# Kernel optimization log

Measured on AMD Instinct MI355X. Metric: run time of the kernel, lower is better.

The kernel has to match this reference:

```python
import jax, jax.numpy as jnp
import numpy as np

B, S, L, D, M = 32, 256, 64, 100, 20  # batch, n_sentences, max_sentence_len, embed_dim, n_memories


def setup_inputs() -> dict:
    key = jax.random.key(0)
    ks = jax.random.split(key, 6)
    batch = jax.random.normal(ks[0], (B, S, L, D), dtype=jnp.float32)
    enc_mult = jnp.ones((L, D), dtype=jnp.float32)  # input_encoder_multiplier (init to ones)
    keys = 0.1 * jax.random.normal(ks[1], (M, D), dtype=jnp.float32)
    U = 0.1 * jax.random.normal(ks[2], (D, D), dtype=jnp.float32)  # nn.Linear weight [out,in]
    V = 0.1 * jax.random.normal(ks[3], (D, D), dtype=jnp.float32)
    W = 0.1 * jax.random.normal(ks[4], (D, D), dtype=jnp.float32)
    prelu_a = jnp.ones((), dtype=jnp.float32)  # PReLU(init=1), single shared parameter
    return {"batch": batch, "enc_mult": enc_mult, "keys": keys, "U": U, "V": V, "W": W, "prelu_a": prelu_a}


def reference(batch, enc_mult, keys, U, V, W, prelu_a):
    # Encode: elementwise multiply by learned positional multiplier, sum over words -> [B, S, D]
    enc = (batch * enc_mult).sum(axis=2)

    def prelu(x):
        return jnp.where(x >= 0, x, prelu_a * x)

    # keys @ V.T is step-invariant
    keysV = jnp.einsum('md,ed->me', keys, V)  # [M, D]

    def step(mem, s):  # mem: [B, M, D], s: [B, D]
        memory_gate = jnp.einsum('bd,bmd->bm', s, mem)          # [B, M]
        key_gate = jnp.einsum('bd,md->bm', s, keys)              # [B, M]
        gate = jax.nn.sigmoid(memory_gate + key_gate)            # [B, M]
        cand = prelu(
            jnp.einsum('bmd,ed->bme', mem, U)                    # U(memories)
            + keysV[None, :, :]                                  # V(keys)
            + jnp.einsum('bd,ed->be', s, W)[:, None, :]          # W(sentence), broadcast over M
        )
        mem = mem + cand * gate[:, :, None]
        mem = mem / jnp.linalg.norm(mem, axis=2, keepdims=True)  # L2 normalize each memory slot
        return mem, None

    mem0 = jnp.broadcast_to(keys[None, :, :], (B, M, D))  # memories init = keys repeated per batch
    mem_final, _ = jax.lax.scan(step, mem0, jnp.swapaxes(enc, 0, 1))  # scan over sentences
    return mem_final
```

## Files before the change

### kernel.cpp

```cpp
#include <hip/hip_runtime.h>


typedef float v2f __attribute__((ext_vector_type(2)));

__global__ __launch_bounds__(320) void encode_k(
    const float* __restrict__ batch,
    const float* __restrict__ encm,
    float* __restrict__ enc)
{
    __shared__ float prod[6400];
    __shared__ float part[200];
    const int t = threadIdx.x;
    const int row = blockIdx.x;
    const float4* rb = (const float4*)batch + (size_t)row * 1600;
    const float4* e4 = (const float4*)encm;
    float4* p4 = (float4*)prod;
    #pragma unroll
    for (int i = 0; i < 5; ++i) {
        const int idx = i * 320 + t;
        float4 x = rb[idx];
        float4 mu = e4[idx];
        float4 p;
        p.x = x.x * mu.x; p.y = x.y * mu.y; p.z = x.z * mu.z; p.w = x.w * mu.w;
        p4[idx] = p;
    }
    __syncthreads();
    if (t < 200) {
        const int c = (t < 100) ? t : (t - 100);
        const int l0 = (t < 100) ? 0 : 32;
        float s0 = 0.f, s1 = 0.f;
        #pragma unroll
        for (int l = 0; l < 32; l += 2) {
            s0 += prod[(l0 + l) * 100 + c];
            s1 += prod[(l0 + l + 1) * 100 + c];
        }
        part[t] = s0 + s1;
    }
    __syncthreads();
    if (t < 100) enc[(size_t)row * 100 + t] = part[t] + part[100 + t];
}

__global__ void prep_k(const float* __restrict__ W,
                       const float* __restrict__ keys,
                       float* __restrict__ T)
{
    const int d = blockIdx.x;
    const int e = threadIdx.x;
    float v = 0.f;
    if (e < 100) v = W[e * 100 + d];
    else if (e < 120) v = keys[(e - 100) * 100 + d];
    T[d * 128 + e] = v;
}

__global__ __launch_bounds__(128) void project_k(
    const float* __restrict__ enc,
    const float* __restrict__ T,
    float* __restrict__ sWp,
    float* __restrict__ kg)
{
    __shared__ float encS[400];
    const int t = threadIdx.x;
    const int row0 = blockIdx.x * 4;
    if (t < 100) ((float4*)encS)[t] = ((const float4*)(enc + (size_t)row0 * 100))[t];
    __syncthreads();
    float a0 = 0.f, a1 = 0.f, a2 = 0.f, a3 = 0.f;
    #pragma unroll 4
    for (int d = 0; d < 100; ++d) {
        const float w = T[d * 128 + t];
        a0 += w * encS[d];
        a1 += w * encS[100 + d];
        a2 += w * encS[200 + d];
        a3 += w * encS[300 + d];
    }
    if (t < 100) {
        sWp[(size_t)row0 * 100 + t]       = a0;
        sWp[(size_t)(row0 + 1) * 100 + t] = a1;
        sWp[(size_t)(row0 + 2) * 100 + t] = a2;
        sWp[(size_t)(row0 + 3) * 100 + t] = a3;
    } else if (t < 120) {
        const int m = t - 100;
        kg[(size_t)row0 * 20 + m]       = a0;
        kg[(size_t)(row0 + 1) * 20 + m] = a1;
        kg[(size_t)(row0 + 2) * 20 + m] = a2;
        kg[(size_t)(row0 + 3) * 20 + m] = a3;
    }
}

template <int CTRL>
__device__ __forceinline__ float dpp_add_f(float x) {
    int s = __builtin_amdgcn_update_dpp(0, __float_as_int(x), CTRL, 0xF, 0xF, true);
    return x + __int_as_float(s);
}
__device__ __forceinline__ float lane63(float x) {
    return __int_as_float(__builtin_amdgcn_readlane(__float_as_int(x), 63));
}
#define DPP6(v) v = dpp_add_f<0x111>(v); v = dpp_add_f<0x112>(v); v = dpp_add_f<0x114>(v); \
                v = dpp_add_f<0x118>(v); v = dpp_add_f<0x142>(v); v = dpp_add_f<0x143>(v);

#define CAND_STORE(C0, C1) { cbuf[lane] = (C0); cbuf[64 + lane] = (C1); }

#define MATVEC_READ(RES)                                                \
    {                                                                   \
        v2f A0 = {0.f, 0.f}, A1 = {0.f, 0.f};                           \
        v2f A2 = {0.f, 0.f}, A3 = {0.f, 0.f};                           \
        _Pragma("unroll")                                               \
        for (int j = 0; j < 25; ++j) {                                  \
            float4 cc = cbuf4[j];                                       \
            v2f clo = {cc.x, cc.y};                                     \
            v2f chi = {cc.z, cc.w};                                     \
            A0 = __builtin_elementwise_fma(UE0[2 * j],     clo, A0);    \
            A1 = __builtin_elementwise_fma(UE0[2 * j + 1], chi, A1);    \
            A2 = __builtin_elementwise_fma(UE1[2 * j],     clo, A2);    \
            A3 = __builtin_elementwise_fma(UE1[2 * j + 1], chi, A3);    \
        }                                                               \
        v2f sA = A0 + A1, sB = A2 + A3;                                 \
        RES.x = sA.x + sA.y;                                            \
        RES.y = sB.x + sB.y;                                            \
    }

__global__ __attribute__((amdgpu_waves_per_eu(1, 1))) __launch_bounds__(64)
void entnet_scan(
    const float* __restrict__ enc,
    const float* __restrict__ sWp,
    const float* __restrict__ kg,
    const float* __restrict__ keys,
    const float* __restrict__ U,
    const float* __restrict__ V,
    const float* __restrict__ paPtr,
    float* __restrict__ out)
{
    __shared__ float4 cbuf4[32];
    float* cbuf = (float*)cbuf4;
    const int lane = threadIdx.x;
    const int xcd = blockIdx.x & 7;
    const int gg  = blockIdx.x >> 3;
    const int b = xcd * 4 + gg / 20;
    const int m = gg % 20;
    const bool hi = (lane < 36);
    const float h = hi ? 1.f : 0.f;
    const int e0 = lane;
    const int e1 = hi ? (64 + lane) : 99;
    const float pa = paPtr[0];

    v2f UE0[50], UE1[50];
    {
        const float4* u0 = (const float4*)(U + e0 * 100);
        const float4* u1 = (const float4*)(U + e1 * 100);
        #pragma unroll
        for (int k = 0; k < 25; ++k) {
            float4 a = u0[k], c = u1[k];
            UE0[2 * k]     = (v2f){a.x, a.y};
            UE0[2 * k + 1] = (v2f){a.z, a.w};
            UE1[2 * k]     = (v2f){c.x, c.y};
            UE1[2 * k + 1] = (v2f){c.z, c.w};
        }
    }

    float kv0 = 0.f, kv1 = 0.f;
    {
        const float4* km = (const float4*)(keys + m * 100);
        const float4* v0 = (const float4*)(V + e0 * 100);
        const float4* v1 = (const float4*)(V + e1 * 100);
        #pragma unroll
        for (int k = 0; k < 25; ++k) {
            float4 kk = km[k], a = v0[k], c = v1[k];
            kv0 += a.x * kk.x + a.y * kk.y + a.z * kk.z + a.w * kk.w;
            kv1 += c.x * kk.x + c.y * kk.y + c.z * kk.z + c.w * kk.w;
        }
    }
    const float k0 = keys[m * 100 + e0];
    const float k1 = h * keys[m * 100 + e1];
    float nm0 = k0, nm1 = k1;

    v2f P;
    CAND_STORE(k0, k1);
    MATVEC_READ(P);

    float nq = k0 * k0 + k1 * k1;
    DPP6(nq)
    float nsq = lane63(nq);
    float rn = 1.f;

    const float* encRow = enc + (size_t)b * 25600;
    const float* sWRow  = sWp + (size_t)b * 25600;
    const float* kgRow  = kg + (size_t)b * 5120 + m;

    float sw0 = sWRow[e0], sw1 = sWRow[e1];
    float g;
    {
        const float sv0 = encRow[e0], sv1 = encRow[e1];
        const float kg0 = kgRow[0];
        float q1 = sv0 * nm0 + sv1 * nm1;
        DPP6(q1)
        const float Q1 = lane63(q1);
        g = 1.f / (1.f + __expf(-(Q1 + kg0)));
    }

    for (int step = 0; step < 256; ++step) {
        const int nxt = (step < 255 ? step + 1 : 255);
        const float nsv0 = encRow[nxt * 100 + e0], nsv1 = encRow[nxt * 100 + e1];
        const float nsw0 = sWRow[nxt * 100 + e0], nsw1 = sWRow[nxt * 100 + e1];
        const float nkg  = kgRow[nxt * 20];

        const float x0 = rn * P.x + kv0 + sw0;
        const float x1 = rn * P.y + kv1 + sw1;
        float c0 = (x0 >= 0.f) ? x0 : pa * x0;
        float c1 = (x1 >= 0.f) ? x1 : pa * x1;
        c1 *= h;

        CAND_STORE(c0, c1);

        float q3 = nm0 * c0 + nm1 * c1;
        float p4 = c0 * c0 + c1 * c1;
        #define RND2(C) q3 = dpp_add_f<C>(q3); p4 = dpp_add_f<C>(p4);
        RND2(0x111) RND2(0x112) RND2(0x114) RND2(0x118) RND2(0x142) RND2(0x143)
        #undef RND2

        v2f Q;
        MATVEC_READ(Q);

        const float Q3 = lane63(q3);
        const float P4 = lane63(p4);
        const float n2 = nsq + 2.f * (g * rn) * Q3 + g * g * P4;
        const float rnn = rsqrtf(n2);
        nsq = 1.f;

        nm0 = rn * nm0 + g * c0;
        nm1 = rn * nm1 + g * c1;
        P.x = rn * P.x + g * Q.x;
        P.y = rn * P.y + g * Q.y;

        float q1 = nsv0 * nm0 + nsv1 * nm1;
        DPP6(q1)
        const float Q1 = lane63(q1);
        g = 1.f / (1.f + __expf(-(rnn * Q1 + nkg)));

        rn = rnn;
        sw0 = nsw0; sw1 = nsw1;
    }
    float* orow = out + (size_t)(b * 20 + m) * 100;
    orow[e0] = nm0 * rn;
    if (hi) orow[e1] = nm1 * rn;
}

extern "C" void kernel_launch(void* const* d_in, const int* in_sizes, int n_in,
                              void* d_out, int out_size, void* d_ws, size_t ws_size,
                              hipStream_t stream) {
    const float* batch = (const float*)d_in[0];
    const float* encm  = (const float*)d_in[1];
    const float* keys  = (const float*)d_in[2];
    const float* U     = (const float*)d_in[3];
    const float* V     = (const float*)d_in[4];
    const float* W     = (const float*)d_in[5];
    const float* pa    = (const float*)d_in[6];
    float* out = (float*)d_out;

    float* enc = (float*)d_ws;
    float* sWp = enc + 819200;
    float* kgb = sWp + 819200;
    float* T   = kgb + 163840;

    encode_k<<<8192, 320, 0, stream>>>(batch, encm, enc);
    prep_k<<<100, 128, 0, stream>>>(W, keys, T);
    project_k<<<2048, 128, 0, stream>>>(enc, T, sWp, kgb);
    entnet_scan<<<640, 64, 0, stream>>>(enc, sWp, kgb, keys, U, V, pa, out);
}
```

Before: 491.6 us.

## Process two memory slots per wave in scan kernel to halve block count

Each scan wave now carries two independent memory slots (m and m+10) instead of one. The U rows held in registers are reused for both matvecs, and the two independent dependency chains interleave, which hides the latency of DPP reductions and LDS accesses. The grid shrinks from 640 to 320 single-wave blocks. On 256 CUs that removes the partial second wave of blocks, but each wave does twice the work per step, so the serial chain length per wave goes up.

```diff
diff --git a/kernel.cpp b/kernel.cpp
--- a/kernel.cpp
+++ b/kernel.cpp
@@ -97,25 +97,29 @@
 #define DPP6(v) v = dpp_add_f<0x111>(v); v = dpp_add_f<0x112>(v); v = dpp_add_f<0x114>(v); \
                 v = dpp_add_f<0x118>(v); v = dpp_add_f<0x142>(v); v = dpp_add_f<0x143>(v);
 
-#define CAND_STORE(C0, C1) { cbuf[lane] = (C0); cbuf[64 + lane] = (C1); }
-
-#define MATVEC_READ(RES)                                                \
+#define MATVEC2(RA, RB)                                                 \
     {                                                                   \
-        v2f A0 = {0.f, 0.f}, A1 = {0.f, 0.f};                           \
-        v2f A2 = {0.f, 0.f}, A3 = {0.f, 0.f};                           \
+        v2f A0 = {0.f,0.f}, A1 = {0.f,0.f}, A2 = {0.f,0.f}, A3 = {0.f,0.f}; \
+        v2f B0 = {0.f,0.f}, B1 = {0.f,0.f}, B2 = {0.f,0.f}, B3 = {0.f,0.f}; \
         _Pragma("unroll")                                               \
         for (int j = 0; j < 25; ++j) {                                  \
-            float4 cc = cbuf4[j];                                       \
-            v2f clo = {cc.x, cc.y};                                     \
-            v2f chi = {cc.z, cc.w};                                     \
-            A0 = __builtin_elementwise_fma(UE0[2 * j],     clo, A0);    \
-            A1 = __builtin_elementwise_fma(UE0[2 * j + 1], chi, A1);    \
-            A2 = __builtin_elementwise_fma(UE1[2 * j],     clo, A2);    \
-            A3 = __builtin_elementwise_fma(UE1[2 * j + 1], chi, A3);    \
+            float4 ca = cbufA4[j];                                      \
+            float4 cb = cbufB4[j];                                      \
+            v2f calo = {ca.x, ca.y}, cahi = {ca.z, ca.w};               \
+            v2f cblo = {cb.x, cb.y}, cbhi = {cb.z, cb.w};               \
+            A0 = __builtin_elementwise_fma(UE0[2 * j],     calo, A0);   \
+            A1 = __builtin_elementwise_fma(UE0[2 * j + 1], cahi, A1);   \
+            A2 = __builtin_elementwise_fma(UE1[2 * j],     calo, A2);   \
+            A3 = __builtin_elementwise_fma(UE1[2 * j + 1], cahi, A3);   \
+            B0 = __builtin_elementwise_fma(UE0[2 * j],     cblo, B0);   \
+            B1 = __builtin_elementwise_fma(UE0[2 * j + 1], cbhi, B1);   \
+            B2 = __builtin_elementwise_fma(UE1[2 * j],     cblo, B2);   \
+            B3 = __builtin_elementwise_fma(UE1[2 * j + 1], cbhi, B3);   \
         }                                                               \
         v2f sA = A0 + A1, sB = A2 + A3;                                 \
-        RES.x = sA.x + sA.y;                                            \
-        RES.y = sB.x + sB.y;                                            \
+        RA.x = sA.x + sA.y;  RA.y = sB.x + sB.y;                        \
+        v2f tA = B0 + B1, tB = B2 + B3;                                 \
+        RB.x = tA.x + tA.y;  RB.y = tB.x + tB.y;                        \
     }
 
 __global__ __attribute__((amdgpu_waves_per_eu(1, 1))) __launch_bounds__(64)
@@ -129,13 +133,16 @@
     const float* __restrict__ paPtr,
     float* __restrict__ out)
 {
-    __shared__ float4 cbuf4[32];
-    float* cbuf = (float*)cbuf4;
+    __shared__ float4 cbufA4[32];
+    __shared__ float4 cbufB4[32];
+    float* cbufA = (float*)cbufA4;
+    float* cbufB = (float*)cbufB4;
     const int lane = threadIdx.x;
     const int xcd = blockIdx.x & 7;
     const int gg  = blockIdx.x >> 3;
-    const int b = xcd * 4 + gg / 20;
-    const int m = gg % 20;
+    const int b  = xcd * 4 + gg / 10;
+    const int mA = gg % 10;
+    const int mB = mA + 10;
     const bool hi = (lane < 36);
     const float h = hi ? 1.f : 0.f;
     const int e0 = lane;
@@ -156,91 +163,132 @@
         }
     }
 
-    float kv0 = 0.f, kv1 = 0.f;
+    float kvA0 = 0.f, kvA1 = 0.f, kvB0 = 0.f, kvB1 = 0.f;
     {
-        const float4* km = (const float4*)(keys + m * 100);
+        const float4* kmA = (const float4*)(keys + mA * 100);
+        const float4* kmB = (const float4*)(keys + mB * 100);
         const float4* v0 = (const float4*)(V + e0 * 100);
         const float4* v1 = (const float4*)(V + e1 * 100);
         #pragma unroll
         for (int k = 0; k < 25; ++k) {
-            float4 kk = km[k], a = v0[k], c = v1[k];
-            kv0 += a.x * kk.x + a.y * kk.y + a.z * kk.z + a.w * kk.w;
-            kv1 += c.x * kk.x + c.y * kk.y + c.z * kk.z + c.w * kk.w;
+            float4 a = v0[k], c = v1[k], ka = kmA[k], kb = kmB[k];
+            kvA0 += a.x * ka.x + a.y * ka.y + a.z * ka.z + a.w * ka.w;
+            kvA1 += c.x * ka.x + c.y * ka.y + c.z * ka.z + c.w * ka.w;
+            kvB0 += a.x * kb.x + a.y * kb.y + a.z * kb.z + a.w * kb.w;
+            kvB1 += c.x * kb.x + c.y * kb.y + c.z * kb.z + c.w * kb.w;
         }
     }
-    const float k0 = keys[m * 100 + e0];
-    const float k1 = h * keys[m * 100 + e1];
-    float nm0 = k0, nm1 = k1;
-
-    v2f P;
-    CAND_STORE(k0, k1);
-    MATVEC_READ(P);
-
-    float nq = k0 * k0 + k1 * k1;
-    DPP6(nq)
-    float nsq = lane63(nq);
-    float rn = 1.f;
+    const float k0A = keys[mA * 100 + e0];
+    const float k1A = h * keys[mA * 100 + e1];
+    const float k0B = keys[mB * 100 + e0];
+    const float k1B = h * keys[mB * 100 + e1];
+    float nmA0 = k0A, nmA1 = k1A;
+    float nmB0 = k0B, nmB1 = k1B;
+
+    v2f PA, PB;
+    cbufA[lane] = k0A; cbufA[64 + lane] = k1A;
+    cbufB[lane] = k0B; cbufB[64 + lane] = k1B;
+    MATVEC2(PA, PB);
+
+    float nqA = k0A * k0A + k1A * k1A;
+    float nqB = k0B * k0B + k1B * k1B;
+    #define RND2I(C) nqA = dpp_add_f<C>(nqA); nqB = dpp_add_f<C>(nqB);
+    RND2I(0x111) RND2I(0x112) RND2I(0x114) RND2I(0x118) RND2I(0x142) RND2I(0x143)
+    #undef RND2I
+    float nsqA = lane63(nqA);
+    float nsqB = lane63(nqB);
+    float rnA = 1.f, rnB = 1.f;
 
     const float* encRow = enc + (size_t)b * 25600;
     const float* sWRow  = sWp + (size_t)b * 25600;
-    const float* kgRow  = kg + (size_t)b * 5120 + m;
+    const float* kgRowA = kg + (size_t)b * 5120 + mA;
+    const float* kgRowB = kg + (size_t)b * 5120 + mB;
 
     float sw0 = sWRow[e0], sw1 = sWRow[e1];
-    float g;
+    float gA, gB;
     {
         const float sv0 = encRow[e0], sv1 = encRow[e1];
-        const float kg0 = kgRow[0];
-        float q1 = sv0 * nm0 + sv1 * nm1;
-        DPP6(q1)
-        const float Q1 = lane63(q1);
-        g = 1.f / (1.f + __expf(-(Q1 + kg0)));
+        const float kgA0 = kgRowA[0];
+        const float kgB0 = kgRowB[0];
+        float q1A = sv0 * nmA0 + sv1 * nmA1;
+        float q1B = sv0 * nmB0 + sv1 * nmB1;
+        #define RND2G(C) q1A = dpp_add_f<C>(q1A); q1B = dpp_add_f<C>(q1B);
+        RND2G(0x111) RND2G(0x112) RND2G(0x114) RND2G(0x118) RND2G(0x142) RND2G(0x143)
+        #undef RND2G
+        gA = 1.f / (1.f + __expf(-(lane63(q1A) + kgA0)));
+        gB = 1.f / (1.f + __expf(-(lane63(q1B) + kgB0)));
     }
 
     for (int step = 0; step < 256; ++step) {
         const int nxt = (step < 255 ? step + 1 : 255);
         const float nsv0 = encRow[nxt * 100 + e0], nsv1 = encRow[nxt * 100 + e1];
         const float nsw0 = sWRow[nxt * 100 + e0], nsw1 = sWRow[nxt * 100 + e1];
-        const float nkg  = kgRow[nxt * 20];
-
-        const float x0 = rn * P.x + kv0 + sw0;
-        const float x1 = rn * P.y + kv1 + sw1;
-        float c0 = (x0 >= 0.f) ? x0 : pa * x0;
-        float c1 = (x1 >= 0.f) ? x1 : pa * x1;
-        c1 *= h;
-
-        CAND_STORE(c0, c1);
-
-        float q3 = nm0 * c0 + nm1 * c1;
-        float p4 = c0 * c0 + c1 * c1;
-        #define RND2(C) q3 = dpp_add_f<C>(q3); p4 = dpp_add_f<C>(p4);
+        const float nkgA = kgRowA[nxt * 20];
+        const float nkgB = kgRowB[nxt * 20];
+
+        const float xA0 = rnA * PA.x + kvA0 + sw0;
+        const float xA1 = rnA * PA.y + kvA1 + sw1;
+        const float xB0 = rnB * PB.x + kvB0 + sw0;
+        const float xB1 = rnB * PB.y + kvB1 + sw1;
+        float cA0 = (xA0 >= 0.f) ? xA0 : pa * xA0;
+        float cA1 = (xA1 >= 0.f) ? xA1 : pa * xA1;
+        float cB0 = (xB0 >= 0.f) ? xB0 : pa * xB0;
+        float cB1 = (xB1 >= 0.f) ? xB1 : pa * xB1;
+        cA1 *= h; cB1 *= h;
+
+        cbufA[lane] = cA0; cbufA[64 + lane] = cA1;
+        cbufB[lane] = cB0; cbufB[64 + lane] = cB1;
+
+        float q3A = nmA0 * cA0 + nmA1 * cA1;
+        float p4A = cA0 * cA0 + cA1 * cA1;
+        float q3B = nmB0 * cB0 + nmB1 * cB1;
+        float p4B = cB0 * cB0 + cB1 * cB1;
+        #define RND4(C) q3A = dpp_add_f<C>(q3A); p4A = dpp_add_f<C>(p4A); \
+                        q3B = dpp_add_f<C>(q3B); p4B = dpp_add_f<C>(p4B);
+        RND4(0x111) RND4(0x112) RND4(0x114) RND4(0x118) RND4(0x142) RND4(0x143)
+        #undef RND4
+
+        v2f QA, QB;
+        MATVEC2(QA, QB);
+
+        const float Q3A = lane63(q3A);
+        const float P4A = lane63(p4A);
+        const float Q3B = lane63(q3B);
+        const float P4B = lane63(p4B);
+        const float n2A = nsqA + 2.f * (gA * rnA) * Q3A + gA * gA * P4A;
+        const float n2B = nsqB + 2.f * (gB * rnB) * Q3B + gB * gB * P4B;
+        const float rnnA = rsqrtf(n2A);
+        const float rnnB = rsqrtf(n2B);
+        nsqA = 1.f; nsqB = 1.f;
+
+        nmA0 = rnA * nmA0 + gA * cA0;
+        nmA1 = rnA * nmA1 + gA * cA1;
+        nmB0 = rnB * nmB0 + gB * cB0;
+        nmB1 = rnB * nmB1 + gB * cB1;
+        PA.x = rnA * PA.x + gA * QA.x;
+        PA.y = rnA * PA.y + gA * QA.y;
+        PB.x = rnB * PB.x + gB * QB.x;
+        PB.y = rnB * PB.y + gB * QB.y;
+
+        float q1A = nsv0 * nmA0 + nsv1 * nmA1;
+        float q1B = nsv0 * nmB0 + nsv1 * nmB1;
+        #define RND2(C) q1A = dpp_add_f<C>(q1A); q1B = dpp_add_f<C>(q1B);
         RND2(0x111) RND2(0x112) RND2(0x114) RND2(0x118) RND2(0x142) RND2(0x143)
         #undef RND2
-
-        v2f Q;
-        MATVEC_READ(Q);
-
-        const float Q3 = lane63(q3);
-        const float P4 = lane63(p4);
-        const float n2 = nsq + 2.f * (g * rn) * Q3 + g * g * P4;
-        const float rnn = rsqrtf(n2);
-        nsq = 1.f;
-
-        nm0 = rn * nm0 + g * c0;
-        nm1 = rn * nm1 + g * c1;
-        P.x = rn * P.x + g * Q.x;
-        P.y = rn * P.y + g * Q.y;
-
-        float q1 = nsv0 * nm0 + nsv1 * nm1;
-        DPP6(q1)
-        const float Q1 = lane63(q1);
-        g = 1.f / (1.f + __expf(-(rnn * Q1 + nkg)));
-
-        rn = rnn;
+        gA = 1.f / (1.f + __expf(-(rnnA * lane63(q1A) + nkgA)));
+        gB = 1.f / (1.f + __expf(-(rnnB * lane63(q1B) + nkgB)));
+
+        rnA = rnnA; rnB = rnnB;
         sw0 = nsw0; sw1 = nsw1;
     }
-    float* orow = out + (size_t)(b * 20 + m) * 100;
-    orow[e0] = nm0 * rn;
-    if (hi) orow[e1] = nm1 * rn;
+    float* orowA = out + (size_t)(b * 20 + mA) * 100;
+    float* orowB = out + (size_t)(b * 20 + mB) * 100;
+    orowA[e0] = nmA0 * rnA;
+    orowB[e0] = nmB0 * rnB;
+    if (hi) {
+        orowA[e1] = nmA1 * rnA;
+        orowB[e1] = nmB1 * rnB;
+    }
 }
 
 extern "C" void kernel_launch(void* const* d_in, const int* in_sizes, int n_in,
@@ -263,5 +311,5 @@
     encode_k<<<8192, 320, 0, stream>>>(batch, encm, enc);
     prep_k<<<100, 128, 0, stream>>>(W, keys, T);
     project_k<<<2048, 128, 0, stream>>>(enc, T, sWp, kgb);
-    entnet_scan<<<640, 64, 0, stream>>>(enc, sWp, kgb, keys, U, V, pa, out);
-}
+    entnet_scan<<<320, 64, 0, stream>>>(enc, sWp, kgb, keys, U, V, pa, out);
+}
```

Measured after the change: 892.2 us. 81.5% more time.

## Split scan per memory slot across two wavefronts with double-buffered LDS

Applied to the files above, without the earlier changes.

The sequential scan kernel now uses 128 threads (two wavefronts) per (batch, memory) slot instead of one wavefront holding two elements per lane. Each thread owns one output dimension and half the U matvec registers. Cross-wave reductions go through a double-buffered LDS slot with one __syncthreads per step. The next-step gate dot product is folded into the same reduction algebraically, which removes a separate DPP chain from the critical path. In exchange each step pays a block barrier, and per-thread register pressure drops, which also lets the waves-per-EU constraint go.

```diff
diff --git a/kernel.cpp b/kernel.cpp
--- a/kernel.cpp
+++ b/kernel.cpp
@@ -91,35 +91,30 @@
     int s = __builtin_amdgcn_update_dpp(0, __float_as_int(x), CTRL, 0xF, 0xF, true);
     return x + __int_as_float(s);
 }
-__device__ __forceinline__ float lane63(float x) {
-    return __int_as_float(__builtin_amdgcn_readlane(__float_as_int(x), 63));
-}
 #define DPP6(v) v = dpp_add_f<0x111>(v); v = dpp_add_f<0x112>(v); v = dpp_add_f<0x114>(v); \
                 v = dpp_add_f<0x118>(v); v = dpp_add_f<0x142>(v); v = dpp_add_f<0x143>(v);
 
-#define CAND_STORE(C0, C1) { cbuf[lane] = (C0); cbuf[64 + lane] = (C1); }
-
-#define MATVEC_READ(RES)                                                \
+#define MATVEC(QOUT, CBPTR)                                             \
     {                                                                   \
-        v2f A0 = {0.f, 0.f}, A1 = {0.f, 0.f};                           \
-        v2f A2 = {0.f, 0.f}, A3 = {0.f, 0.f};                           \
+        v2f A0 = {0.f,0.f}, A1 = {0.f,0.f};                             \
+        v2f A2 = {0.f,0.f}, A3 = {0.f,0.f};                             \
         _Pragma("unroll")                                               \
         for (int j = 0; j < 25; ++j) {                                  \
-            float4 cc = cbuf4[j];                                       \
-            v2f clo = {cc.x, cc.y};                                     \
-            v2f chi = {cc.z, cc.w};                                     \
-            A0 = __builtin_elementwise_fma(UE0[2 * j],     clo, A0);    \
-            A1 = __builtin_elementwise_fma(UE0[2 * j + 1], chi, A1);    \
-            A2 = __builtin_elementwise_fma(UE1[2 * j],     clo, A2);    \
-            A3 = __builtin_elementwise_fma(UE1[2 * j + 1], chi, A3);    \
+            float4 cc = (CBPTR)[j];                                     \
+            v2f lo = {cc.x, cc.y}, hi4 = {cc.z, cc.w};                  \
+            if (j & 1) {                                                \
+                A2 = __builtin_elementwise_fma(UE[2*j],   lo,  A2);     \
+                A3 = __builtin_elementwise_fma(UE[2*j+1], hi4, A3);     \
+            } else {                                                    \
+                A0 = __builtin_elementwise_fma(UE[2*j],   lo,  A0);     \
+                A1 = __builtin_elementwise_fma(UE[2*j+1], hi4, A1);     \
+            }                                                           \
         }                                                               \
-        v2f sA = A0 + A1, sB = A2 + A3;                                 \
-        RES.x = sA.x + sA.y;                                            \
-        RES.y = sB.x + sB.y;                                            \
-    }
-
-__global__ __attribute__((amdgpu_waves_per_eu(1, 1))) __launch_bounds__(64)
-void entnet_scan(
+        v2f S = (A0 + A1) + (A2 + A3);                                  \
+        QOUT = S.x + S.y;                                               \
+    }
+
+__global__ __launch_bounds__(128) void entnet_scan(
     const float* __restrict__ enc,
     const float* __restrict__ sWp,
     const float* __restrict__ kg,
@@ -129,118 +124,121 @@
     const float* __restrict__ paPtr,
     float* __restrict__ out)
 {
-    __shared__ float4 cbuf4[32];
+    __shared__ float4 cbuf4[2][32];
+    __shared__ float4 red[2][2];
     float* cbuf = (float*)cbuf4;
-    const int lane = threadIdx.x;
+    const int tid  = threadIdx.x;
+    const int lane = tid & 63;
+    const int wid  = tid >> 6;
     const int xcd = blockIdx.x & 7;
     const int gg  = blockIdx.x >> 3;
     const int b = xcd * 4 + gg / 20;
     const int m = gg % 20;
-    const bool hi = (lane < 36);
-    const float h = hi ? 1.f : 0.f;
-    const int e0 = lane;
-    const int e1 = hi ? (64 + lane) : 99;
+    const bool act = (tid < 100);
+    const float h = act ? 1.f : 0.f;
+    const int e = act ? tid : 99;
     const float pa = paPtr[0];
 
-    v2f UE0[50], UE1[50];
-    {
-        const float4* u0 = (const float4*)(U + e0 * 100);
-        const float4* u1 = (const float4*)(U + e1 * 100);
+    v2f UE[50];
+    {
+        const float4* u = (const float4*)(U + e * 100);
         #pragma unroll
         for (int k = 0; k < 25; ++k) {
-            float4 a = u0[k], c = u1[k];
-            UE0[2 * k]     = (v2f){a.x, a.y};
-            UE0[2 * k + 1] = (v2f){a.z, a.w};
-            UE1[2 * k]     = (v2f){c.x, c.y};
-            UE1[2 * k + 1] = (v2f){c.z, c.w};
-        }
-    }
-
-    float kv0 = 0.f, kv1 = 0.f;
+            float4 a = u[k];
+            UE[2*k]   = (v2f){a.x, a.y};
+            UE[2*k+1] = (v2f){a.z, a.w};
+        }
+    }
+
+    float kv = 0.f;
     {
         const float4* km = (const float4*)(keys + m * 100);
-        const float4* v0 = (const float4*)(V + e0 * 100);
-        const float4* v1 = (const float4*)(V + e1 * 100);
+        const float4* vv = (const float4*)(V + e * 100);
         #pragma unroll
         for (int k = 0; k < 25; ++k) {
-            float4 kk = km[k], a = v0[k], c = v1[k];
-            kv0 += a.x * kk.x + a.y * kk.y + a.z * kk.z + a.w * kk.w;
-            kv1 += c.x * kk.x + c.y * kk.y + c.z * kk.z + c.w * kk.w;
-        }
-    }
-    const float k0 = keys[m * 100 + e0];
-    const float k1 = h * keys[m * 100 + e1];
-    float nm0 = k0, nm1 = k1;
-
-    v2f P;
-    CAND_STORE(k0, k1);
-    MATVEC_READ(P);
-
-    float nq = k0 * k0 + k1 * k1;
-    DPP6(nq)
-    float nsq = lane63(nq);
-    float rn = 1.f;
+            float4 a = vv[k], kk = km[k];
+            kv += a.x * kk.x + a.y * kk.y + a.z * kk.z + a.w * kk.w;
+        }
+    }
 
     const float* encRow = enc + (size_t)b * 25600;
     const float* sWRow  = sWp + (size_t)b * 25600;
     const float* kgRow  = kg + (size_t)b * 5120 + m;
 
-    float sw0 = sWRow[e0], sw1 = sWRow[e1];
-    float g;
-    {
-        const float sv0 = encRow[e0], sv1 = encRow[e1];
-        const float kg0 = kgRow[0];
-        float q1 = sv0 * nm0 + sv1 * nm1;
-        DPP6(q1)
-        const float Q1 = lane63(q1);
-        g = 1.f / (1.f + __expf(-(Q1 + kg0)));
-    }
+    const float k0 = keys[m * 100 + e];
+    float nm = k0;
+
+    cbuf[128 + tid] = k0;
+    float nq  = h * k0 * k0;
+    const float sv0 = encRow[e];
+    float q1i = h * sv0 * k0;
+    DPP6(nq) DPP6(q1i)
+    if (lane == 63) red[1][wid] = (float4){nq, q1i, 0.f, 0.f};
+    __syncthreads();
+
+    float P;
+    {
+        const float4* cb1 = (const float4*)(&cbuf[128]);
+        MATVEC(P, cb1);
+    }
+    float nsq, g;
+    {
+        float4 r0 = red[1][0], r1 = red[1][1];
+        nsq = r0.x + r1.x;
+        const float Q1 = r0.y + r1.y;
+        g = 1.f / (1.f + __expf(-(Q1 + kgRow[0])));
+    }
+    float rn = 1.f;
+    float sw = sWRow[e];
 
     for (int step = 0; step < 256; ++step) {
         const int nxt = (step < 255 ? step + 1 : 255);
-        const float nsv0 = encRow[nxt * 100 + e0], nsv1 = encRow[nxt * 100 + e1];
-        const float nsw0 = sWRow[nxt * 100 + e0], nsw1 = sWRow[nxt * 100 + e1];
-        const float nkg  = kgRow[nxt * 20];
-
-        const float x0 = rn * P.x + kv0 + sw0;
-        const float x1 = rn * P.y + kv1 + sw1;
-        float c0 = (x0 >= 0.f) ? x0 : pa * x0;
-        float c1 = (x1 >= 0.f) ? x1 : pa * x1;
-        c1 *= h;
-
-        CAND_STORE(c0, c1);
-
-        float q3 = nm0 * c0 + nm1 * c1;
-        float p4 = c0 * c0 + c1 * c1;
-        #define RND2(C) q3 = dpp_add_f<C>(q3); p4 = dpp_add_f<C>(p4);
-        RND2(0x111) RND2(0x112) RND2(0x114) RND2(0x118) RND2(0x142) RND2(0x143)
-        #undef RND2
-
-        v2f Q;
-        MATVEC_READ(Q);
-
-        const float Q3 = lane63(q3);
-        const float P4 = lane63(p4);
-        const float n2 = nsq + 2.f * (g * rn) * Q3 + g * g * P4;
+        const float nsv = encRow[nxt * 100 + e];
+        const float nsw = sWRow[nxt * 100 + e];
+        const float nkg = kgRow[nxt * 20];
+
+        const float x = rn * P + kv + sw;
+        const float c = (x >= 0.f) ? x : pa * x;
+        const int bi = step & 1;
+        cbuf[bi * 128 + tid] = c;
+
+        float q3  = h * nm * c;
+        float p4  = h * c * c;
+        float q0  = h * nsv * nm;
+        float r1v = h * nsv * c;
+        #define RND4(C) q3 = dpp_add_f<C>(q3); p4 = dpp_add_f<C>(p4); \
+                        q0 = dpp_add_f<C>(q0); r1v = dpp_add_f<C>(r1v);
+        RND4(0x111) RND4(0x112) RND4(0x114) RND4(0x118) RND4(0x142) RND4(0x143)
+        #undef RND4
+        if (lane == 63) red[bi][wid] = (float4){q3, p4, q0, r1v};
+        __syncthreads();
+
+        float Q;
+        {
+            const float4* cb = (const float4*)(&cbuf[bi * 128]);
+            MATVEC(Q, cb);
+        }
+
+        float4 ra = red[bi][0], rb = red[bi][1];
+        const float Q3 = ra.x + rb.x;
+        const float P4 = ra.y + rb.y;
+        const float Q0 = ra.z + rb.z;
+        const float R1 = ra.w + rb.w;
+
+        const float n2  = nsq + 2.f * (g * rn) * Q3 + g * g * P4;
         const float rnn = rsqrtf(n2);
         nsq = 1.f;
 
-        nm0 = rn * nm0 + g * c0;
-        nm1 = rn * nm1 + g * c1;
-        P.x = rn * P.x + g * Q.x;
-        P.y = rn * P.y + g * Q.y;
-
-        float q1 = nsv0 * nm0 + nsv1 * nm1;
-        DPP6(q1)
-        const float Q1 = lane63(q1);
+        nm = rn * nm + g * c;
+        P  = rn * P  + g * Q;
+
+        const float Q1 = rn * Q0 + g * R1;
         g = 1.f / (1.f + __expf(-(rnn * Q1 + nkg)));
 
         rn = rnn;
-        sw0 = nsw0; sw1 = nsw1;
-    }
-    float* orow = out + (size_t)(b * 20 + m) * 100;
-    orow[e0] = nm0 * rn;
-    if (hi) orow[e1] = nm1 * rn;
+        sw = nsw;
+    }
+    if (act) out[(size_t)(b * 20 + m) * 100 + tid] = nm * rn;
 }
 
 extern "C" void kernel_launch(void* const* d_in, const int* in_sizes, int n_in,
@@ -263,5 +261,5 @@
     encode_k<<<8192, 320, 0, stream>>>(batch, encm, enc);
     prep_k<<<100, 128, 0, stream>>>(W, keys, T);
     project_k<<<2048, 128, 0, stream>>>(enc, T, sWp, kgb);
-    entnet_scan<<<640, 64, 0, stream>>>(enc, sWp, kgb, keys, U, V, pa, out);
-}
+    entnet_scan<<<640, 128, 0, stream>>>(enc, sWp, kgb, keys, U, V, pa, out);
+}
```

Measured after the change: 531.0 us. +8.0%, slower.
